# Kernel tuning notes

Measured on AMD Instinct MI355X. Metric: run time of the kernel, lower is better.

The kernel has to match this reference:

```python
import jax, jax.numpy as jnp
import numpy as np

N_NODES = 50000
N_EDGES = 800000
D_IN = 128
D_OUT = 128


def setup_inputs() -> dict:
    key = jax.random.key(0)
    k1, k2, k3, k4, k5, k6 = jax.random.split(key, 6)
    x = jax.random.normal(k1, (N_NODES, D_IN), dtype=jnp.float32)
    weight = jax.random.normal(k2, (D_IN, D_OUT), dtype=jnp.float32)
    bias = jax.random.normal(k3, (D_OUT,), dtype=jnp.float32)
    adj_row = jax.random.randint(k4, (N_EDGES,), 0, N_NODES, dtype=jnp.int64)
    adj_col = jax.random.randint(k5, (N_EDGES,), 0, N_NODES, dtype=jnp.int64)
    adj_val = jax.random.uniform(k6, (N_EDGES,), dtype=jnp.float32)
    return {"x": x, "weight": weight, "bias": bias,
            "adj_row": adj_row, "adj_col": adj_col, "adj_val": adj_val}


def reference(x, weight, bias, adj_row, adj_col, adj_val):
    # support = x @ W  -- dense GEMM [N, D_in] x [D_in, D_out]
    support = jnp.matmul(x, weight)
    # spmm(adj, support): out[i] = sum_e adj_val[e] * support[adj_col[e]] for adj_row[e]==i
    messages = support[adj_col] * adj_val[:, None]          # [E, D_out]
    output = jax.ops.segment_sum(messages, adj_row, num_segments=x.shape[0])
    return output + bias
```

## Files before the change

### kernel.cpp

```cpp
#include <hip/hip_runtime.h>

#define D 128
#define ELL_CAP 64
#define EPT 8

typedef __attribute__((ext_vector_type(8))) short short8;
typedef __attribute__((ext_vector_type(4))) float floatx4;
typedef unsigned int uint;
typedef unsigned short ushort;

__device__ inline short f2bf(float f) {
  unsigned u = __float_as_uint(f);
  u += 0x7FFF + ((u >> 16) & 1);
  return (short)(u >> 16);
}

__global__ __launch_bounds__(256) void gemm_scatter_kernel(
    const float* __restrict__ x, const float* __restrict__ w,
    ushort* __restrict__ support, int n_nodes, int gemm_blocks,
    const int* __restrict__ adj_row, const int* __restrict__ adj_col,
    const float* __restrict__ adj_val, int* __restrict__ cnt,
    uint* __restrict__ ell, int n_edges, int range_size) {
  __shared__ short sWA[2 * 8 * 64 * 8];
  const int tid = threadIdx.x;

  if ((int)blockIdx.x < gemm_blocks) {
    const int wid = tid >> 6;
    const int lane = tid & 63;
    const int quad = lane >> 4;
    const int node = blockIdx.x * 64 + wid * 16 + (lane & 15);
    const bool ok = (node < n_nodes);

    floatx4 acc[8];
#pragma unroll
    for (int mt = 0; mt < 8; ++mt) acc[mt] = (floatx4){0.f, 0.f, 0.f, 0.f};

#pragma unroll
    for (int kt2 = 0; kt2 < 4; kt2 += 2) {
      if (kt2) __syncthreads();
      for (int s = tid; s < 1024; s += 256) {
        int ktmt = s >> 6, ls = s & 63;
        int kt = kt2 + (ktmt >> 3);
        int kb = kt * 32 + (ls >> 4) * 8;
        int m = (ktmt & 7) * 16 + (ls & 15);
        short8 frag;
#pragma unroll
        for (int j = 0; j < 8; ++j) frag[j] = f2bf(w[(kb + j) * D + m]);
        *(short8*)&sWA[s * 8] = frag;
      }
      __syncthreads();

#pragma unroll
      for (int ktoff = 0; ktoff < 2; ++ktoff) {
        const int kt = kt2 + ktoff;
        short8 bfr = (short8){0, 0, 0, 0, 0, 0, 0, 0};
        if (ok) {
          const float4 v0 = *(const float4*)&x[(size_t)node * D + kt * 32 + quad * 8];
          const float4 v1 = *(const float4*)&x[(size_t)node * D + kt * 32 + quad * 8 + 4];
          bfr = (short8){f2bf(v0.x), f2bf(v0.y), f2bf(v0.z), f2bf(v0.w),
                         f2bf(v1.x), f2bf(v1.y), f2bf(v1.z), f2bf(v1.w)};
        }
#pragma unroll
        for (int mt = 0; mt < 8; ++mt) {
          short8 a = *(const short8*)&sWA[((ktoff * 8 + mt) * 64 + lane) * 8];
          acc[mt] = __builtin_amdgcn_mfma_f32_16x16x32_bf16(a, bfr, acc[mt], 0, 0, 0);
        }
      }
    }

    if (ok) {
#pragma unroll
      for (int mt = 0; mt < 8; ++mt) {
        uint lo = ((uint)(ushort)f2bf(acc[mt][1]) << 16) | (ushort)f2bf(acc[mt][0]);
        uint hi = ((uint)(ushort)f2bf(acc[mt][3]) << 16) | (ushort)f2bf(acc[mt][2]);
        *(uint2*)&support[(size_t)node * D + mt * 16 + quad * 4] = make_uint2(lo, hi);
      }
    }
  } else {
    const int b = blockIdx.x - gemm_blocks;
    const int g = b & 7;
    const int c = b >> 3;
    const int lo = g * range_size, hi = lo + range_size;
    const int base = c * (256 * EPT) + tid * EPT;

    if (base + EPT <= n_edges) {
      int4 r0 = *(const int4*)&adj_row[base];
      int4 r1 = *(const int4*)&adj_row[base + 4];
      int4 c0 = *(const int4*)&adj_col[base];
      int4 c1 = *(const int4*)&adj_col[base + 4];
      float4 v0 = *(const float4*)&adj_val[base];
      float4 v1 = *(const float4*)&adj_val[base + 4];
      int rr[EPT] = {r0.x, r0.y, r0.z, r0.w, r1.x, r1.y, r1.z, r1.w};
      int cc[EPT] = {c0.x, c0.y, c0.z, c0.w, c1.x, c1.y, c1.z, c1.w};
      float vv[EPT] = {v0.x, v0.y, v0.z, v0.w, v1.x, v1.y, v1.z, v1.w};
#pragma unroll
      for (int u = 0; u < EPT; ++u) {
        int r = rr[u];
        if (r >= lo && r < hi) {
          int pos = atomicAdd(&cnt[r], 1);
          if (pos < ELL_CAP)
            ell[(size_t)r * ELL_CAP + pos] = ((uint)cc[u] << 16) | (ushort)f2bf(vv[u]);
        }
      }
    } else {
      for (int u = 0; u < EPT; ++u) {
        int e = base + u;
        if (e >= n_edges) break;
        int r = adj_row[e];
        if (r >= lo && r < hi) {
          int pos = atomicAdd(&cnt[r], 1);
          if (pos < ELL_CAP)
            ell[(size_t)r * ELL_CAP + pos] = ((uint)adj_col[e] << 16) | (ushort)f2bf(adj_val[e]);
        }
      }
    }
  }
}

__global__ __launch_bounds__(256) void spmm_ell_kernel(const int* __restrict__ cnt,
                                                       const uint* __restrict__ ell,
                                                       const uint* __restrict__ sup,
                                                       const float* __restrict__ bias,
                                                       float* __restrict__ out,
                                                       int n_rows) {
  const int wave = (int)((blockIdx.x * 256 + threadIdx.x) >> 6);
  const int lane = threadIdx.x & 63;
  const int qtr = lane >> 4;
  const int hl = lane & 15;
  const int r = wave * 4 + qtr;
  if (wave * 4 >= n_rows) return;

  int n = 0;
  if (r < n_rows) n = cnt[r];
  if (n > ELL_CAP) n = ELL_CAP;

  uint4 ent = make_uint4(0, 0, 0, 0);
  if (r < n_rows) {
    ent = *(const uint4*)&ell[(size_t)r * ELL_CAP + hl * 4];
    ent.x = (hl * 4 + 0 < n) ? ent.x : 0u;
    ent.y = (hl * 4 + 1 < n) ? ent.y : 0u;
    ent.z = (hl * 4 + 2 < n) ? ent.z : 0u;
    ent.w = (hl * 4 + 3 < n) ? ent.w : 0u;
  }

  int nmax = n, t;
  t = __shfl_xor(nmax, 16); if (t > nmax) nmax = t;
  t = __shfl_xor(nmax, 32); if (t > nmax) nmax = t;
  const int m = (nmax + 7) & ~7;

  float a0 = 0.f, a1 = 0.f, a2 = 0.f, a3 = 0.f;
  float a4 = 0.f, a5 = 0.f, a6 = 0.f, a7 = 0.f;
  const int qbase = lane & 0x30;
  for (int j = 0; j < m; j += 8) {
    uint e[8];
    uint4 s[8];
#pragma unroll
    for (int u = 0; u < 8; ++u) {
      int src = qbase + ((j + u) >> 2);
      uint val = (u & 3) == 0 ? ent.x : (u & 3) == 1 ? ent.y : (u & 3) == 2 ? ent.z : ent.w;
      e[u] = __shfl(val, src);
    }
#pragma unroll
    for (int u = 0; u < 8; ++u)
      s[u] = *(const uint4*)&sup[(size_t)(e[u] >> 16) * 64 + hl * 4];
#pragma unroll
    for (int u = 0; u < 8; ++u) {
      float wv = __uint_as_float(e[u] << 16);
      a0 = fmaf(wv, __uint_as_float(s[u].x << 16), a0);
      a1 = fmaf(wv, __uint_as_float(s[u].x & 0xffff0000u), a1);
      a2 = fmaf(wv, __uint_as_float(s[u].y << 16), a2);
      a3 = fmaf(wv, __uint_as_float(s[u].y & 0xffff0000u), a3);
      a4 = fmaf(wv, __uint_as_float(s[u].z << 16), a4);
      a5 = fmaf(wv, __uint_as_float(s[u].z & 0xffff0000u), a5);
      a6 = fmaf(wv, __uint_as_float(s[u].w << 16), a6);
      a7 = fmaf(wv, __uint_as_float(s[u].w & 0xffff0000u), a7);
    }
  }

  if (r < n_rows) {
    float4 b0 = *(const float4*)&bias[hl * 8];
    float4 b1 = *(const float4*)&bias[hl * 8 + 4];
    *(float4*)&out[(size_t)r * D + hl * 8] =
        make_float4(b0.x + a0, b0.y + a1, b0.z + a2, b0.w + a3);
    *(float4*)&out[(size_t)r * D + hl * 8 + 4] =
        make_float4(b1.x + a4, b1.y + a5, b1.z + a6, b1.w + a7);
  }
}

extern "C" void kernel_launch(void* const* d_in, const int* in_sizes, int n_in,
                              void* d_out, int out_size, void* d_ws, size_t ws_size,
                              hipStream_t stream) {
  const float* x       = (const float*)d_in[0];
  const float* w       = (const float*)d_in[1];
  const float* bias    = (const float*)d_in[2];
  const int*   adj_row = (const int*)d_in[3];
  const int*   adj_col = (const int*)d_in[4];
  const float* adj_val = (const float*)d_in[5];

  const int n_nodes = in_sizes[0] / D;
  const int n_edges = in_sizes[3];
  float* out = (float*)d_out;

  char* ws = (char*)d_ws;
  ushort* support = (ushort*)ws; ws += ((size_t)n_nodes * D * 2 + 15) & ~15ull;
  int*    row_cnt = (int*)ws;    ws += ((size_t)n_nodes * 4 + 15) & ~15ull;
  uint*   ell     = (uint*)ws;   ws += (size_t)n_nodes * ELL_CAP * 4;

  hipMemsetAsync(row_cnt, 0, (size_t)n_nodes * 4, stream);

  const int gemm_blocks = (n_nodes + 63) / 64;
  const int range_size = (n_nodes + 7) / 8;
  const int chunks = (n_edges + 256 * EPT - 1) / (256 * EPT);
  gemm_scatter_kernel<<<gemm_blocks + chunks * 8, 256, 0, stream>>>(
      x, w, support, n_nodes, gemm_blocks,
      adj_row, adj_col, adj_val, row_cnt, ell, n_edges, range_size);

  int waves = (n_nodes + 3) / 4;
  int spmm_blocks = (waves + 3) / 4;
  spmm_ell_kernel<<<spmm_blocks, 256, 0, stream>>>(row_cnt, ell, (const uint*)support,
                                                   bias, out, n_nodes);
}
```

Before: 155.3 us.

## Bind scatter row ranges to hardware XCD with per-XCD ticket work queues

Scatter blocks now read the hardware XCC_ID and take the row range that belongs to their XCD, instead of deriving it from the block index. Each block pulls edge chunks from a per-XCD atomic ticket counter until all chunks are consumed. The row-counter atomics are relaxed with workgroup scope. The aim is to keep each row range's count and ELL traffic inside one XCD's L2 and to avoid cross-die coherence costs on the atomics. The risks: correctness now depends on every XCD receiving at least one scatter block, and on workgroup-scope atomics staying coherent within one L2; each chunk also costs an extra ticket atomic and two barriers.

```diff
diff --git a/kernel.cpp b/kernel.cpp
--- a/kernel.cpp
+++ b/kernel.cpp
@@ -3,6 +3,7 @@
 #define D 128
 #define ELL_CAP 64
 #define EPT 8
+#define NXCD 8
 
 typedef __attribute__((ext_vector_type(8))) short short8;
 typedef __attribute__((ext_vector_type(4))) float floatx4;
@@ -13,6 +14,12 @@
   unsigned u = __float_as_uint(f);
   u += 0x7FFF + ((u >> 16) & 1);
   return (short)(u >> 16);
+}
+
+__device__ inline int xcc_id() {
+  int x;
+  asm volatile("s_getreg_b32 %0, hwreg(HW_REG_XCC_ID)" : "=s"(x));
+  return x & (NXCD - 1);
 }
 
 __global__ __launch_bounds__(256) void gemm_scatter_kernel(
@@ -20,7 +27,8 @@
     ushort* __restrict__ support, int n_nodes, int gemm_blocks,
     const int* __restrict__ adj_row, const int* __restrict__ adj_col,
     const float* __restrict__ adj_val, int* __restrict__ cnt,
-    uint* __restrict__ ell, int n_edges, int range_size) {
+    uint* __restrict__ ell, int n_edges, int range_size,
+    int* __restrict__ ticket, int n_chunks) {
   __shared__ short sWA[2 * 8 * 64 * 8];
   const int tid = threadIdx.x;
 
@@ -77,40 +85,49 @@
       }
     }
   } else {
-    const int b = blockIdx.x - gemm_blocks;
-    const int g = b & 7;
-    const int c = b >> 3;
+    const int g = xcc_id();
     const int lo = g * range_size, hi = lo + range_size;
-    const int base = c * (256 * EPT) + tid * EPT;
-
-    if (base + EPT <= n_edges) {
-      int4 r0 = *(const int4*)&adj_row[base];
-      int4 r1 = *(const int4*)&adj_row[base + 4];
-      int4 c0 = *(const int4*)&adj_col[base];
-      int4 c1 = *(const int4*)&adj_col[base + 4];
-      float4 v0 = *(const float4*)&adj_val[base];
-      float4 v1 = *(const float4*)&adj_val[base + 4];
-      int rr[EPT] = {r0.x, r0.y, r0.z, r0.w, r1.x, r1.y, r1.z, r1.w};
-      int cc[EPT] = {c0.x, c0.y, c0.z, c0.w, c1.x, c1.y, c1.z, c1.w};
-      float vv[EPT] = {v0.x, v0.y, v0.z, v0.w, v1.x, v1.y, v1.z, v1.w};
-#pragma unroll
-      for (int u = 0; u < EPT; ++u) {
-        int r = rr[u];
-        if (r >= lo && r < hi) {
-          int pos = atomicAdd(&cnt[r], 1);
-          if (pos < ELL_CAP)
-            ell[(size_t)r * ELL_CAP + pos] = ((uint)cc[u] << 16) | (ushort)f2bf(vv[u]);
-        }
-      }
-    } else {
-      for (int u = 0; u < EPT; ++u) {
-        int e = base + u;
-        if (e >= n_edges) break;
-        int r = adj_row[e];
-        if (r >= lo && r < hi) {
-          int pos = atomicAdd(&cnt[r], 1);
-          if (pos < ELL_CAP)
-            ell[(size_t)r * ELL_CAP + pos] = ((uint)adj_col[e] << 16) | (ushort)f2bf(adj_val[e]);
+    int* sC = (int*)sWA;
+
+    for (;;) {
+      if (tid == 0) sC[0] = atomicAdd(ticket + g, 1);
+      __syncthreads();
+      const int c = sC[0];
+      __syncthreads();
+      if (c >= n_chunks) return;
+
+      const int base = c * (256 * EPT) + tid * EPT;
+      if (base + EPT <= n_edges) {
+        int4 r0 = *(const int4*)&adj_row[base];
+        int4 r1 = *(const int4*)&adj_row[base + 4];
+        int4 c0 = *(const int4*)&adj_col[base];
+        int4 c1 = *(const int4*)&adj_col[base + 4];
+        float4 v0 = *(const float4*)&adj_val[base];
+        float4 v1 = *(const float4*)&adj_val[base + 4];
+        int rr[EPT] = {r0.x, r0.y, r0.z, r0.w, r1.x, r1.y, r1.z, r1.w};
+        int cc[EPT] = {c0.x, c0.y, c0.z, c0.w, c1.x, c1.y, c1.z, c1.w};
+        float vv[EPT] = {v0.x, v0.y, v0.z, v0.w, v1.x, v1.y, v1.z, v1.w};
+#pragma unroll
+        for (int u = 0; u < EPT; ++u) {
+          int r = rr[u];
+          if (r >= lo && r < hi) {
+            int pos = __hip_atomic_fetch_add(&cnt[r], 1, __ATOMIC_RELAXED,
+                                             __HIP_MEMORY_SCOPE_WORKGROUP);
+            if (pos < ELL_CAP)
+              ell[(size_t)r * ELL_CAP + pos] = ((uint)cc[u] << 16) | (ushort)f2bf(vv[u]);
+          }
+        }
+      } else {
+        for (int u = 0; u < EPT; ++u) {
+          int e = base + u;
+          if (e >= n_edges) break;
+          int r = adj_row[e];
+          if (r >= lo && r < hi) {
+            int pos = __hip_atomic_fetch_add(&cnt[r], 1, __ATOMIC_RELAXED,
+                                             __HIP_MEMORY_SCOPE_WORKGROUP);
+            if (pos < ELL_CAP)
+              ell[(size_t)r * ELL_CAP + pos] = ((uint)adj_col[e] << 16) | (ushort)f2bf(adj_val[e]);
+          }
         }
       }
     }
@@ -204,16 +221,18 @@
   char* ws = (char*)d_ws;
   ushort* support = (ushort*)ws; ws += ((size_t)n_nodes * D * 2 + 15) & ~15ull;
   int*    row_cnt = (int*)ws;    ws += ((size_t)n_nodes * 4 + 15) & ~15ull;
+  int*    ticket  = (int*)ws;    ws += 32;
   uint*   ell     = (uint*)ws;   ws += (size_t)n_nodes * ELL_CAP * 4;
 
-  hipMemsetAsync(row_cnt, 0, (size_t)n_nodes * 4, stream);
+  hipMemsetAsync(row_cnt, 0, (size_t)n_nodes * 4 + 32, stream);
 
   const int gemm_blocks = (n_nodes + 63) / 64;
-  const int range_size = (n_nodes + 7) / 8;
+  const int range_size = (n_nodes + NXCD - 1) / NXCD;
   const int chunks = (n_edges + 256 * EPT - 1) / (256 * EPT);
-  gemm_scatter_kernel<<<gemm_blocks + chunks * 8, 256, 0, stream>>>(
+  gemm_scatter_kernel<<<gemm_blocks + chunks * NXCD, 256, 0, stream>>>(
       x, w, support, n_nodes, gemm_blocks,
-      adj_row, adj_col, adj_val, row_cnt, ell, n_edges, range_size);
+      adj_row, adj_col, adj_val, row_cnt, ell, n_edges, range_size,
+      ticket, chunks);
 
   int waves = (n_nodes + 3) / 4;
   int spmm_blocks = (waves + 3) / 4;
```

Result: slower. 197.5 us (+27.1%).
